# Optimization experiments

Hardware: AMD Instinct MI355X
Metric: run time of the kernel (lower is better)

Reference implementation:

```python
import jax, jax.numpy as jnp
import numpy as np

N_NODES = 100000
N_EDGES = 600000
IN_C, HID_C, OUT_C = 128, 128, 64


def gcn_conv(x, W, b, src, dst, n_nodes):
    """PyG GCNConv: out = D^{-1/2} (A + I) D^{-1/2} X W + b (symmetric norm, self-loops)."""
    h = x @ W  # [N, C_out] transform first (as PyG does)
    # add self loops
    loop = jnp.arange(n_nodes, dtype=src.dtype)
    s = jnp.concatenate([src, loop])
    d = jnp.concatenate([dst, loop])
    # degree over targets (edge weight = 1)
    deg = jax.ops.segment_sum(jnp.ones_like(d, dtype=h.dtype), d, num_segments=n_nodes)
    dinv = jnp.where(deg > 0, jax.lax.rsqrt(deg), 0.0)
    norm = dinv[s] * dinv[d]  # [E+N]
    msg = h[s] * norm[:, None]  # gather + scale
    out = jax.ops.segment_sum(msg, d, num_segments=n_nodes)  # scatter-add
    return out + b


def setup_inputs() -> dict:
    key = jax.random.key(0)
    k1, k2, k3, k4, k5 = jax.random.split(key, 5)
    x = jax.random.normal(k1, (N_NODES, IN_C), dtype=jnp.float32)
    src = jax.random.randint(k2, (N_EDGES,), 0, N_NODES, dtype=jnp.int32)
    dst = jax.random.randint(k3, (N_EDGES,), 0, N_NODES, dtype=jnp.int32)
    # Glorot-style init for conv weights, zero bias (PyG defaults)
    W1 = jax.random.normal(k4, (IN_C, HID_C), dtype=jnp.float32) * (1.0 / np.sqrt(IN_C))
    W2 = jax.random.normal(k5, (HID_C, OUT_C), dtype=jnp.float32) * (1.0 / np.sqrt(HID_C))
    b1 = jnp.zeros((HID_C,), dtype=jnp.float32)
    b2 = jnp.zeros((OUT_C,), dtype=jnp.float32)
    return {"x": x, "W1": W1, "b1": b1, "W2": W2, "b2": b2, "src": src, "dst": dst}


def reference(x, W1, b1, W2, b2, src, dst):
    h = gcn_conv(x, W1, b1, src, dst, N_NODES)
    h = jax.nn.relu(h)
    out = gcn_conv(h, W2, b2, src, dst, N_NODES)
    return out
```

## Files before the change

### kernel.cpp

```cpp
#include <hip/hip_runtime.h>
#include <math.h>


typedef __bf16 bf16x8 __attribute__((ext_vector_type(8)));
typedef float f32x4 __attribute__((ext_vector_type(4)));

constexpr int CAP = 32;

union ABu {
  unsigned short u16[8];
  uint4 u4;
  bf16x8 v;
};

__device__ inline unsigned short f2bf(float f) {
  unsigned u = __float_as_uint(f);
  return (unsigned short)((u + 0x7fffu + ((u >> 16) & 1u)) >> 16);
}

__device__ inline void unpack8(uint4 v, float* f) {
  f[0] = __uint_as_float(v.x << 16);
  f[1] = __uint_as_float(v.x & 0xffff0000u);
  f[2] = __uint_as_float(v.y << 16);
  f[3] = __uint_as_float(v.y & 0xffff0000u);
  f[4] = __uint_as_float(v.z << 16);
  f[5] = __uint_as_float(v.z & 0xffff0000u);
  f[6] = __uint_as_float(v.w << 16);
  f[7] = __uint_as_float(v.w & 0xffff0000u);
}

__device__ inline uint4 pack8(const float* a) {
  uint4 o;
  o.x = (unsigned)f2bf(a[0]) | ((unsigned)f2bf(a[1]) << 16);
  o.y = (unsigned)f2bf(a[2]) | ((unsigned)f2bf(a[3]) << 16);
  o.z = (unsigned)f2bf(a[4]) | ((unsigned)f2bf(a[5]) << 16);
  o.w = (unsigned)f2bf(a[6]) | ((unsigned)f2bf(a[7]) << 16);
  return o;
}

__global__ __launch_bounds__(256) void k_pre(const float* __restrict__ W1,
                                             const float* __restrict__ W2,
                                             unsigned short* __restrict__ Wb1,
                                             unsigned short* __restrict__ Wb2,
                                             int* __restrict__ counts, int n) {
  constexpr int CONV_BLOCKS = (128 * 128 + 128 * 64) / 256;
  if (blockIdx.x < CONV_BLOCKS) {
    int idx = blockIdx.x * 256 + threadIdx.x;
    if (idx < 128 * 128) {
      int k = idx >> 7, c = idx & 127;
      Wb1[(((k >> 3) << 7) + c) * 8 + (k & 7)] = f2bf(W1[idx]);
    } else {
      int j = idx - 128 * 128;
      int k = j >> 6, c = j & 63;
      Wb2[(((k >> 3) << 6) + c) * 8 + (k & 7)] = f2bf(W2[j]);
    }
    return;
  }
  int i = (blockIdx.x - CONV_BLOCKS) * 256 + threadIdx.x;
  if (i < n) counts[i] = 0;
}


__device__ inline void slot_body(const int* __restrict__ src,
                                 const int* __restrict__ dst,
                                 int* __restrict__ counts,
                                 int* __restrict__ eslot, int E, int bid) {
  int base = (bid * 256 + (int)threadIdx.x) * 8;
  if (base + 7 < E) {
    int4 d0 = *(const int4*)(dst + base);
    int4 d1 = *(const int4*)(dst + base + 4);
    int4 s0 = *(const int4*)(src + base);
    int4 s1 = *(const int4*)(src + base + 4);
    int r0 = atomicAdd(&counts[d0.x], 1);
    int r1 = atomicAdd(&counts[d0.y], 1);
    int r2 = atomicAdd(&counts[d0.z], 1);
    int r3 = atomicAdd(&counts[d0.w], 1);
    int r4 = atomicAdd(&counts[d1.x], 1);
    int r5 = atomicAdd(&counts[d1.y], 1);
    int r6 = atomicAdd(&counts[d1.z], 1);
    int r7 = atomicAdd(&counts[d1.w], 1);
    r0 = r0 < CAP - 1 ? r0 : CAP - 1;
    r1 = r1 < CAP - 1 ? r1 : CAP - 1;
    r2 = r2 < CAP - 1 ? r2 : CAP - 1;
    r3 = r3 < CAP - 1 ? r3 : CAP - 1;
    r4 = r4 < CAP - 1 ? r4 : CAP - 1;
    r5 = r5 < CAP - 1 ? r5 : CAP - 1;
    r6 = r6 < CAP - 1 ? r6 : CAP - 1;
    r7 = r7 < CAP - 1 ? r7 : CAP - 1;
    eslot[(size_t)d0.x * CAP + r0] = s0.x;
    eslot[(size_t)d0.y * CAP + r1] = s0.y;
    eslot[(size_t)d0.z * CAP + r2] = s0.z;
    eslot[(size_t)d0.w * CAP + r3] = s0.w;
    eslot[(size_t)d1.x * CAP + r4] = s1.x;
    eslot[(size_t)d1.y * CAP + r5] = s1.y;
    eslot[(size_t)d1.z * CAP + r6] = s1.z;
    eslot[(size_t)d1.w * CAP + r7] = s1.w;
  } else {
    for (int e = base; e < E; ++e) {
      int dd = dst[e];
      int r = atomicAdd(&counts[dd], 1);
      r = r < CAP - 1 ? r : CAP - 1;
      eslot[(size_t)dd * CAP + r] = src[e];
    }
  }
}

__device__ inline void gemm1_body(const float* __restrict__ X,
                                  const unsigned short* __restrict__ Wb,
                                  unsigned short* __restrict__ Cb, int M,
                                  int rowblk) {
  constexpr int K = 128, N = 128, NT = N / 16, KS = K / 32;
  const int tid = threadIdx.x;
  const int wave = tid >> 6;
  const int lane = tid & 63;
  const int q = lane >> 4;
  const int l15 = lane & 15;
  const int row0 = rowblk * 64 + wave * 16;
  const int rowA = row0 + l15;

  f32x4 zero = {0.0f, 0.0f, 0.0f, 0.0f};
  f32x4 acc[NT];
#pragma unroll
  for (int t = 0; t < NT; ++t) acc[t] = zero;

#pragma unroll
  for (int kk = 0; kk < KS; ++kk) {
    ABu a;
    float4 f0 = make_float4(0.f, 0.f, 0.f, 0.f);
    float4 f1 = make_float4(0.f, 0.f, 0.f, 0.f);
    if (rowA < M) {
      const float4* ap = (const float4*)(X + (size_t)rowA * K + kk * 32 + q * 8);
      f0 = ap[0];
      f1 = ap[1];
    }
    a.u16[0] = f2bf(f0.x); a.u16[1] = f2bf(f0.y);
    a.u16[2] = f2bf(f0.z); a.u16[3] = f2bf(f0.w);
    a.u16[4] = f2bf(f1.x); a.u16[5] = f2bf(f1.y);
    a.u16[6] = f2bf(f1.z); a.u16[7] = f2bf(f1.w);
#pragma unroll
    for (int nt = 0; nt < NT; ++nt) {
      ABu b;
      b.u4 = *(const uint4*)(Wb + ((size_t)(kk * 4 + q) * N + nt * 16 + l15) * 8);
      acc[nt] = __builtin_amdgcn_mfma_f32_16x16x32_bf16(a.v, b.v, acc[nt], 0, 0, 0);
    }
  }

#pragma unroll
  for (int v = 0; v < 4; ++v) {
    int row = row0 + q * 4 + v;
    if (row < M) {
#pragma unroll
      for (int nt = 0; nt < NT; ++nt)
        Cb[(size_t)row * N + nt * 16 + l15] = f2bf(acc[nt][v]);
    }
  }
}

__global__ __launch_bounds__(256) void k_slot_gemm1(
    const int* __restrict__ src, const int* __restrict__ dst,
    int* __restrict__ counts, int* __restrict__ eslot, int E, int EB,
    const float* __restrict__ X, const unsigned short* __restrict__ Wb1,
    unsigned short* __restrict__ h1, int M) {
  if ((int)blockIdx.x < EB)
    slot_body(src, dst, counts, eslot, E, blockIdx.x);
  else
    gemm1_body(X, Wb1, h1, M, blockIdx.x - EB);
}

__global__ __launch_bounds__(256) void k_dinv(const int* __restrict__ counts,
                                              float* __restrict__ dinv, int n) {
  int i = blockIdx.x * 256 + threadIdx.x;
  if (i < n) dinv[i] = rsqrtf((float)(counts[i] + 1));
}

__global__ __launch_bounds__(256) void k_aggemm(const unsigned short* __restrict__ h1,
                                                const float* __restrict__ dinv,
                                                const float* __restrict__ b1,
                                                const int* __restrict__ counts,
                                                const int* __restrict__ eslot,
                                                const unsigned short* __restrict__ Wb2,
                                                unsigned short* __restrict__ h2s,
                                                int n) {
  constexpr int LDA = 136;
  __shared__ unsigned short As[16 * LDA];
  __shared__ float sdinv[16];
  const int tid = threadIdx.x;

  {
    const int nl = tid >> 4;
    const int q = tid & 15;
    const int node = blockIdx.x * 16 + nl;
    float acc[8];
    if (node < n) {
      const uint4* h4 = (const uint4*)h1;
      float di = dinv[node];
      if (q == 0) sdinv[nl] = di;
      unpack8(h4[(size_t)node * 16 + q], acc);
#pragma unroll
      for (int j = 0; j < 8; ++j) acc[j] *= di;

      int cnt = counts[node];
      if (cnt > CAP) cnt = CAP;
      const int* sl = eslot + (size_t)node * CAP;
      if (cnt > 0) {
        int lim = cnt < 16 ? cnt : 16;
        int my_s = sl[q < lim ? q : 0];
        float my_dv = dinv[my_s];
        for (int e = 0; e < lim; e += 8) {
          int idx[8];
          float dv[8];
#pragma unroll
          for (int i = 0; i < 8; ++i) {
            idx[i] = __shfl(my_s, e + i, 16);
            float dl = __shfl(my_dv, e + i, 16);
            dv[i] = (e + i < lim) ? dl : 0.f;
          }
          uint4 rr[8];
#pragma unroll
          for (int i = 0; i < 8; ++i) rr[i] = h4[(size_t)idx[i] * 16 + q];
#pragma unroll
          for (int i = 0; i < 8; ++i) {
            float g[8];
            unpack8(rr[i], g);
#pragma unroll
            for (int j = 0; j < 8; ++j) acc[j] = fmaf(g[j], dv[i], acc[j]);
          }
        }
        if (cnt > 16) {
          int rem = cnt - 16;
          int my_s2 = sl[16 + (q < rem ? q : 0)];
          float my_dv2 = dinv[my_s2];
          for (int e = 0; e < rem; e += 8) {
            int idx[8];
            float dv[8];
#pragma unroll
            for (int i = 0; i < 8; ++i) {
              idx[i] = __shfl(my_s2, e + i, 16);
              float dl = __shfl(my_dv2, e + i, 16);
              dv[i] = (e + i < rem) ? dl : 0.f;
            }
            uint4 rr[8];
#pragma unroll
            for (int i = 0; i < 8; ++i) rr[i] = h4[(size_t)idx[i] * 16 + q];
#pragma unroll
            for (int i = 0; i < 8; ++i) {
              float g[8];
              unpack8(rr[i], g);
#pragma unroll
              for (int j = 0; j < 8; ++j) acc[j] = fmaf(g[j], dv[i], acc[j]);
            }
          }
        }
      }
      const float4* b14 = (const float4*)b1;
      float4 ba = b14[q * 2], bb = b14[q * 2 + 1];
      float bias[8] = {ba.x, ba.y, ba.z, ba.w, bb.x, bb.y, bb.z, bb.w};
#pragma unroll
      for (int i = 0; i < 8; ++i) acc[i] = fmaxf(fmaf(acc[i], di, bias[i]), 0.f);
    } else {
      if (q == 0) sdinv[nl] = 0.f;
#pragma unroll
      for (int i = 0; i < 8; ++i) acc[i] = 0.f;
    }
    *(uint4*)&As[nl * LDA + q * 8] = pack8(acc);
  }
  __syncthreads();

  {
    const int wave = tid >> 6;
    const int lane = tid & 63;
    const int q = lane >> 4;
    const int l15 = lane & 15;
    f32x4 acc = {0.0f, 0.0f, 0.0f, 0.0f};
#pragma unroll
    for (int kk = 0; kk < 4; ++kk) {
      ABu a, b;
      a.u4 = *(const uint4*)&As[l15 * LDA + kk * 32 + q * 8];
      b.u4 = *(const uint4*)(Wb2 + ((size_t)(kk * 4 + q) * 64 + wave * 16 + l15) * 8);
      acc = __builtin_amdgcn_mfma_f32_16x16x32_bf16(a.v, b.v, acc, 0, 0, 0);
    }
#pragma unroll
    for (int v = 0; v < 4; ++v) {
      int rl = q * 4 + v;
      int row = blockIdx.x * 16 + rl;
      if (row < n) h2s[(size_t)row * 64 + wave * 16 + l15] = f2bf(acc[v] * sdinv[rl]);
    }
  }
}

__global__ __launch_bounds__(256) void k_agg2(const unsigned short* __restrict__ h2s,
                                              const float* __restrict__ dinv,
                                              const float* __restrict__ b2,
                                              const int* __restrict__ counts,
                                              const int* __restrict__ eslot,
                                              float* __restrict__ out, int n) {
  constexpr int CQ = 8;
  const int tid = threadIdx.x;
  const int node = blockIdx.x * 32 + tid / CQ;
  const int q = tid % CQ;
  if (node >= n) return;

  const uint4* h4 = (const uint4*)h2s;
  float di = dinv[node];
  float acc[8];
  unpack8(h4[(size_t)node * CQ + q], acc);

  int cnt = counts[node];
  if (cnt > CAP) cnt = CAP;
  const int* sl = eslot + (size_t)node * CAP;
  for (int b = 0; b * 8 < cnt; ++b) {
    int rem = cnt - b * 8;
    int lim = rem < 8 ? rem : 8;
    int my_s = sl[b * 8 + (q < lim ? q : 0)];
    int idx[8];
#pragma unroll
    for (int i = 0; i < 8; ++i) idx[i] = __shfl(my_s, i, 8);
    uint4 rr[8];
#pragma unroll
    for (int i = 0; i < 8; ++i) rr[i] = h4[(size_t)idx[i] * CQ + q];
#pragma unroll
    for (int i = 0; i < 8; ++i) {
      float w = (i < lim) ? 1.f : 0.f;
      float g[8];
      unpack8(rr[i], g);
#pragma unroll
      for (int j = 0; j < 8; ++j) acc[j] = fmaf(g[j], w, acc[j]);
    }
  }

  const float4* b24 = (const float4*)b2;
  float4 ba = b24[q * 2], bb = b24[q * 2 + 1];
  float bias[8] = {ba.x, ba.y, ba.z, ba.w, bb.x, bb.y, bb.z, bb.w};
  float4 o0, o1;
  o0.x = fmaf(acc[0], di, bias[0]);
  o0.y = fmaf(acc[1], di, bias[1]);
  o0.z = fmaf(acc[2], di, bias[2]);
  o0.w = fmaf(acc[3], di, bias[3]);
  o1.x = fmaf(acc[4], di, bias[4]);
  o1.y = fmaf(acc[5], di, bias[5]);
  o1.z = fmaf(acc[6], di, bias[6]);
  o1.w = fmaf(acc[7], di, bias[7]);
  ((float4*)out)[(size_t)node * 16 + q * 2 + 0] = o0;
  ((float4*)out)[(size_t)node * 16 + q * 2 + 1] = o1;
}


extern "C" void kernel_launch(void* const* d_in, const int* in_sizes, int n_in,
                              void* d_out, int out_size, void* d_ws, size_t ws_size,
                              hipStream_t stream) {
  const float* x  = (const float*)d_in[0];
  const float* W1 = (const float*)d_in[1];
  const float* b1 = (const float*)d_in[2];
  const float* W2 = (const float*)d_in[3];
  const float* b2 = (const float*)d_in[4];
  const int* src  = (const int*)d_in[5];
  const int* dst  = (const int*)d_in[6];
  float* out = (float*)d_out;

  constexpr int IN_C = 128, HID_C = 128, OUT_C = 64;
  const int N = in_sizes[0] / IN_C;
  const int E = in_sizes[5];

  char* p = (char*)d_ws;
  auto alloc = [&](size_t bytes) {
    char* r = p;
    p += (bytes + 255) & ~(size_t)255;
    return r;
  };
  float* dinv    = (float*)alloc((size_t)N * 4);
  int*   counts  = (int*)alloc((size_t)N * 4);
  int*   eslot   = (int*)alloc((size_t)N * CAP * 4);
  unsigned short* Wb1 = (unsigned short*)alloc((size_t)IN_C * HID_C * 2);
  unsigned short* Wb2 = (unsigned short*)alloc((size_t)HID_C * OUT_C * 2);
  unsigned short* h1  = (unsigned short*)alloc((size_t)N * HID_C * 2);
  unsigned short* h2s = (unsigned short*)alloc((size_t)N * OUT_C * 2);

  const int T = 256;
  const int EB8 = ((E + 7) / 8 + T - 1) / T;
  const int RB_TOTAL = (N + 63) / 64;
  constexpr int CONV_BLOCKS = (128 * 128 + 128 * 64) / 256;

  k_pre<<<CONV_BLOCKS + (N + T - 1) / T, T, 0, stream>>>(W1, W2, Wb1, Wb2, counts, N);
  k_slot_gemm1<<<EB8 + RB_TOTAL, T, 0, stream>>>(src, dst, counts, eslot, E, EB8,
                                                 x, Wb1, h1, N);
  k_dinv<<<(N + T - 1) / T, T, 0, stream>>>(counts, dinv, N);
  k_aggemm<<<(N + 15) / 16, T, 0, stream>>>(h1, dinv, b1, counts, eslot, Wb2, h2s, N);
  k_agg2<<<(N + 31) / 32, T, 0, stream>>>(h2s, dinv, b2, counts, eslot, out, N);
}
```

Before: 202.5 us.

## Build per-node edge slots with LDS histograms in 128 scanning blocks

Replaces the global-atomic edge bucketing with 128 blocks. Each block owns a contiguous range of destination nodes, scans the whole dst array, and counts edges into a shared-memory histogram using LDS atomics. The same blocks then write counts and dinv directly, which removes the counts zeroing in k_pre and the separate k_dinv launch. The cost is that every scanning block reads the full edge list, so total reads grow about 128-fold and are likely served from L2. That extra traffic may outweigh the savings from avoiding global atomic contention.

```diff
diff --git a/kernel.cpp b/kernel.cpp
--- a/kernel.cpp
+++ b/kernel.cpp
@@ -6,6 +6,7 @@
 typedef float f32x4 __attribute__((ext_vector_type(4)));
 
 constexpr int CAP = 32;
+constexpr int NB_SCAN = 128;
 
 union ABu {
   unsigned short u16[8];
@@ -41,67 +42,78 @@
 __global__ __launch_bounds__(256) void k_pre(const float* __restrict__ W1,
                                              const float* __restrict__ W2,
                                              unsigned short* __restrict__ Wb1,
-                                             unsigned short* __restrict__ Wb2,
-                                             int* __restrict__ counts, int n) {
-  constexpr int CONV_BLOCKS = (128 * 128 + 128 * 64) / 256;
-  if (blockIdx.x < CONV_BLOCKS) {
-    int idx = blockIdx.x * 256 + threadIdx.x;
-    if (idx < 128 * 128) {
-      int k = idx >> 7, c = idx & 127;
-      Wb1[(((k >> 3) << 7) + c) * 8 + (k & 7)] = f2bf(W1[idx]);
-    } else {
-      int j = idx - 128 * 128;
-      int k = j >> 6, c = j & 63;
-      Wb2[(((k >> 3) << 6) + c) * 8 + (k & 7)] = f2bf(W2[j]);
-    }
-    return;
-  }
-  int i = (blockIdx.x - CONV_BLOCKS) * 256 + threadIdx.x;
-  if (i < n) counts[i] = 0;
-}
-
-
-__device__ inline void slot_body(const int* __restrict__ src,
+                                             unsigned short* __restrict__ Wb2) {
+  int idx = blockIdx.x * 256 + threadIdx.x;
+  if (idx < 128 * 128) {
+    int k = idx >> 7, c = idx & 127;
+    Wb1[(((k >> 3) << 7) + c) * 8 + (k & 7)] = f2bf(W1[idx]);
+  } else {
+    int j = idx - 128 * 128;
+    int k = j >> 6, c = j & 63;
+    Wb2[(((k >> 3) << 6) + c) * 8 + (k & 7)] = f2bf(W2[j]);
+  }
+}
+
+
+__device__ inline void scan_body(const int* __restrict__ src,
                                  const int* __restrict__ dst,
                                  int* __restrict__ counts,
-                                 int* __restrict__ eslot, int E, int bid) {
-  int base = (bid * 256 + (int)threadIdx.x) * 8;
-  if (base + 7 < E) {
-    int4 d0 = *(const int4*)(dst + base);
-    int4 d1 = *(const int4*)(dst + base + 4);
-    int4 s0 = *(const int4*)(src + base);
-    int4 s1 = *(const int4*)(src + base + 4);
-    int r0 = atomicAdd(&counts[d0.x], 1);
-    int r1 = atomicAdd(&counts[d0.y], 1);
-    int r2 = atomicAdd(&counts[d0.z], 1);
-    int r3 = atomicAdd(&counts[d0.w], 1);
-    int r4 = atomicAdd(&counts[d1.x], 1);
-    int r5 = atomicAdd(&counts[d1.y], 1);
-    int r6 = atomicAdd(&counts[d1.z], 1);
-    int r7 = atomicAdd(&counts[d1.w], 1);
-    r0 = r0 < CAP - 1 ? r0 : CAP - 1;
-    r1 = r1 < CAP - 1 ? r1 : CAP - 1;
-    r2 = r2 < CAP - 1 ? r2 : CAP - 1;
-    r3 = r3 < CAP - 1 ? r3 : CAP - 1;
-    r4 = r4 < CAP - 1 ? r4 : CAP - 1;
-    r5 = r5 < CAP - 1 ? r5 : CAP - 1;
-    r6 = r6 < CAP - 1 ? r6 : CAP - 1;
-    r7 = r7 < CAP - 1 ? r7 : CAP - 1;
-    eslot[(size_t)d0.x * CAP + r0] = s0.x;
-    eslot[(size_t)d0.y * CAP + r1] = s0.y;
-    eslot[(size_t)d0.z * CAP + r2] = s0.z;
-    eslot[(size_t)d0.w * CAP + r3] = s0.w;
-    eslot[(size_t)d1.x * CAP + r4] = s1.x;
-    eslot[(size_t)d1.y * CAP + r5] = s1.y;
-    eslot[(size_t)d1.z * CAP + r6] = s1.z;
-    eslot[(size_t)d1.w * CAP + r7] = s1.w;
-  } else {
-    for (int e = base; e < E; ++e) {
-      int dd = dst[e];
-      int r = atomicAdd(&counts[dd], 1);
-      r = r < CAP - 1 ? r : CAP - 1;
-      eslot[(size_t)dd * CAP + r] = src[e];
-    }
+                                 float* __restrict__ dinv,
+                                 int* __restrict__ eslot,
+                                 int E, int N, int bid, int* hist) {
+  const int per = (N + NB_SCAN - 1) / NB_SCAN;
+  const int base = bid * per;
+  int lim = N - base;
+  lim = lim < per ? lim : per;
+  if (lim < 0) lim = 0;
+  for (int i = threadIdx.x; i < lim; i += 256) hist[i] = 0;
+  __syncthreads();
+
+  const int4* d4 = (const int4*)dst;
+  const int nv = E >> 2;
+  for (int v = threadIdx.x; v < nv; v += 256) {
+    int4 d = d4[v];
+    int e0 = v << 2;
+    unsigned r;
+    r = (unsigned)(d.x - base);
+    if (r < (unsigned)lim) {
+      int rk = atomicAdd(&hist[r], 1);
+      rk = rk < CAP - 1 ? rk : CAP - 1;
+      eslot[(size_t)d.x * CAP + rk] = src[e0 + 0];
+    }
+    r = (unsigned)(d.y - base);
+    if (r < (unsigned)lim) {
+      int rk = atomicAdd(&hist[r], 1);
+      rk = rk < CAP - 1 ? rk : CAP - 1;
+      eslot[(size_t)d.y * CAP + rk] = src[e0 + 1];
+    }
+    r = (unsigned)(d.z - base);
+    if (r < (unsigned)lim) {
+      int rk = atomicAdd(&hist[r], 1);
+      rk = rk < CAP - 1 ? rk : CAP - 1;
+      eslot[(size_t)d.z * CAP + rk] = src[e0 + 2];
+    }
+    r = (unsigned)(d.w - base);
+    if (r < (unsigned)lim) {
+      int rk = atomicAdd(&hist[r], 1);
+      rk = rk < CAP - 1 ? rk : CAP - 1;
+      eslot[(size_t)d.w * CAP + rk] = src[e0 + 3];
+    }
+  }
+  for (int e = (nv << 2) + (int)threadIdx.x; e < E; e += 256) {
+    int dd = dst[e];
+    unsigned r = (unsigned)(dd - base);
+    if (r < (unsigned)lim) {
+      int rk = atomicAdd(&hist[r], 1);
+      rk = rk < CAP - 1 ? rk : CAP - 1;
+      eslot[(size_t)dd * CAP + rk] = src[e];
+    }
+  }
+  __syncthreads();
+  for (int i = threadIdx.x; i < lim; i += 256) {
+    int c = hist[i];
+    counts[base + i] = c;
+    dinv[base + i] = rsqrtf((float)(c + 1));
   }
 }
 
@@ -156,21 +168,17 @@
   }
 }
 
-__global__ __launch_bounds__(256) void k_slot_gemm1(
+__global__ __launch_bounds__(256) void k_scan_gemm1(
     const int* __restrict__ src, const int* __restrict__ dst,
-    int* __restrict__ counts, int* __restrict__ eslot, int E, int EB,
+    int* __restrict__ counts, float* __restrict__ dinv,
+    int* __restrict__ eslot, int E, int N,
     const float* __restrict__ X, const unsigned short* __restrict__ Wb1,
     unsigned short* __restrict__ h1, int M) {
-  if ((int)blockIdx.x < EB)
-    slot_body(src, dst, counts, eslot, E, blockIdx.x);
+  __shared__ int hist[1024];
+  if ((int)blockIdx.x < NB_SCAN)
+    scan_body(src, dst, counts, dinv, eslot, E, N, blockIdx.x, hist);
   else
-    gemm1_body(X, Wb1, h1, M, blockIdx.x - EB);
-}
-
-__global__ __launch_bounds__(256) void k_dinv(const int* __restrict__ counts,
-                                              float* __restrict__ dinv, int n) {
-  int i = blockIdx.x * 256 + threadIdx.x;
-  if (i < n) dinv[i] = rsqrtf((float)(counts[i] + 1));
+    gemm1_body(X, Wb1, h1, M, blockIdx.x - NB_SCAN);
 }
 
 __global__ __launch_bounds__(256) void k_aggemm(const unsigned short* __restrict__ h1,
@@ -376,14 +384,12 @@
   unsigned short* h2s = (unsigned short*)alloc((size_t)N * OUT_C * 2);
 
   const int T = 256;
-  const int EB8 = ((E + 7) / 8 + T - 1) / T;
   const int RB_TOTAL = (N + 63) / 64;
   constexpr int CONV_BLOCKS = (128 * 128 + 128 * 64) / 256;
 
-  k_pre<<<CONV_BLOCKS + (N + T - 1) / T, T, 0, stream>>>(W1, W2, Wb1, Wb2, counts, N);
-  k_slot_gemm1<<<EB8 + RB_TOTAL, T, 0, stream>>>(src, dst, counts, eslot, E, EB8,
-                                                 x, Wb1, h1, N);
-  k_dinv<<<(N + T - 1) / T, T, 0, stream>>>(counts, dinv, N);
+  k_pre<<<CONV_BLOCKS, T, 0, stream>>>(W1, W2, Wb1, Wb2);
+  k_scan_gemm1<<<NB_SCAN + RB_TOTAL, T, 0, stream>>>(src, dst, counts, dinv, eslot,
+                                                     E, N, x, Wb1, h1, N);
   k_aggemm<<<(N + 15) / 16, T, 0, stream>>>(h1, dinv, b1, counts, eslot, Wb2, h2s, N);
   k_agg2<<<(N + 31) / 32, T, 0, stream>>>(h2s, dinv, b2, counts, eslot, out, N);
 }
```

After: 463.2 us. +128.7%, slower.

## Replace global per-node atomics with two-pass binned edge bucketing

Applied to the files above, without the earlier changes.

Edge slotting no longer uses a global atomic per edge on the per-node counts array. Edges are first bucketed into 1024-node bins using shared-memory histograms plus one global atomic per bin per block. A second kernel then builds each bin's slot lists and degree/dinv with shared-memory atomics. This removes the zeroing of counts and the separate dinv kernel, but adds a pass that writes and re-reads an int2 bin buffer. Bin overflow past CAPB silently drops edges, so bounds clamps were added to the aggregation kernels.

```diff
diff --git a/kernel.cpp b/kernel.cpp
--- a/kernel.cpp
+++ b/kernel.cpp
@@ -6,6 +6,7 @@
 typedef float f32x4 __attribute__((ext_vector_type(4)));
 
 constexpr int CAP = 32;
+constexpr int CAPB = 8192;
 
 union ABu {
   unsigned short u16[8];
@@ -42,65 +43,70 @@
                                              const float* __restrict__ W2,
                                              unsigned short* __restrict__ Wb1,
                                              unsigned short* __restrict__ Wb2,
-                                             int* __restrict__ counts, int n) {
+                                             int* __restrict__ gCur, int nbins) {
   constexpr int CONV_BLOCKS = (128 * 128 + 128 * 64) / 256;
-  if (blockIdx.x < CONV_BLOCKS) {
-    int idx = blockIdx.x * 256 + threadIdx.x;
-    if (idx < 128 * 128) {
-      int k = idx >> 7, c = idx & 127;
-      Wb1[(((k >> 3) << 7) + c) * 8 + (k & 7)] = f2bf(W1[idx]);
-    } else {
-      int j = idx - 128 * 128;
-      int k = j >> 6, c = j & 63;
-      Wb2[(((k >> 3) << 6) + c) * 8 + (k & 7)] = f2bf(W2[j]);
-    }
+  if (blockIdx.x == CONV_BLOCKS) {
+    if ((int)threadIdx.x < nbins) gCur[threadIdx.x] = 0;
     return;
   }
-  int i = (blockIdx.x - CONV_BLOCKS) * 256 + threadIdx.x;
-  if (i < n) counts[i] = 0;
-}
-
-
-__device__ inline void slot_body(const int* __restrict__ src,
+  int idx = blockIdx.x * 256 + threadIdx.x;
+  if (idx < 128 * 128) {
+    int k = idx >> 7, c = idx & 127;
+    Wb1[(((k >> 3) << 7) + c) * 8 + (k & 7)] = f2bf(W1[idx]);
+  } else {
+    int j = idx - 128 * 128;
+    int k = j >> 6, c = j & 63;
+    Wb2[(((k >> 3) << 6) + c) * 8 + (k & 7)] = f2bf(W2[j]);
+  }
+}
+
+
+__device__ inline void binA_body(const int* __restrict__ src,
                                  const int* __restrict__ dst,
-                                 int* __restrict__ counts,
-                                 int* __restrict__ eslot, int E, int bid) {
-  int base = (bid * 256 + (int)threadIdx.x) * 8;
+                                 int* __restrict__ gCur,
+                                 int2* __restrict__ binBuf,
+                                 int E, int nbins, int bid,
+                                 int* bc, int* bbase) {
+  const int tid = threadIdx.x;
+  if (tid < 128) bc[tid] = 0;
+  __syncthreads();
+  int base = (bid * 256 + tid) * 8;
+  int ds[8], ss[8];
+  bool vl[8];
   if (base + 7 < E) {
     int4 d0 = *(const int4*)(dst + base);
     int4 d1 = *(const int4*)(dst + base + 4);
     int4 s0 = *(const int4*)(src + base);
     int4 s1 = *(const int4*)(src + base + 4);
-    int r0 = atomicAdd(&counts[d0.x], 1);
-    int r1 = atomicAdd(&counts[d0.y], 1);
-    int r2 = atomicAdd(&counts[d0.z], 1);
-    int r3 = atomicAdd(&counts[d0.w], 1);
-    int r4 = atomicAdd(&counts[d1.x], 1);
-    int r5 = atomicAdd(&counts[d1.y], 1);
-    int r6 = atomicAdd(&counts[d1.z], 1);
-    int r7 = atomicAdd(&counts[d1.w], 1);
-    r0 = r0 < CAP - 1 ? r0 : CAP - 1;
-    r1 = r1 < CAP - 1 ? r1 : CAP - 1;
-    r2 = r2 < CAP - 1 ? r2 : CAP - 1;
-    r3 = r3 < CAP - 1 ? r3 : CAP - 1;
-    r4 = r4 < CAP - 1 ? r4 : CAP - 1;
-    r5 = r5 < CAP - 1 ? r5 : CAP - 1;
-    r6 = r6 < CAP - 1 ? r6 : CAP - 1;
-    r7 = r7 < CAP - 1 ? r7 : CAP - 1;
-    eslot[(size_t)d0.x * CAP + r0] = s0.x;
-    eslot[(size_t)d0.y * CAP + r1] = s0.y;
-    eslot[(size_t)d0.z * CAP + r2] = s0.z;
-    eslot[(size_t)d0.w * CAP + r3] = s0.w;
-    eslot[(size_t)d1.x * CAP + r4] = s1.x;
-    eslot[(size_t)d1.y * CAP + r5] = s1.y;
-    eslot[(size_t)d1.z * CAP + r6] = s1.z;
-    eslot[(size_t)d1.w * CAP + r7] = s1.w;
+    ds[0] = d0.x; ds[1] = d0.y; ds[2] = d0.z; ds[3] = d0.w;
+    ds[4] = d1.x; ds[5] = d1.y; ds[6] = d1.z; ds[7] = d1.w;
+    ss[0] = s0.x; ss[1] = s0.y; ss[2] = s0.z; ss[3] = s0.w;
+    ss[4] = s1.x; ss[5] = s1.y; ss[6] = s1.z; ss[7] = s1.w;
+#pragma unroll
+    for (int i = 0; i < 8; ++i) vl[i] = true;
   } else {
-    for (int e = base; e < E; ++e) {
-      int dd = dst[e];
-      int r = atomicAdd(&counts[dd], 1);
-      r = r < CAP - 1 ? r : CAP - 1;
-      eslot[(size_t)dd * CAP + r] = src[e];
+#pragma unroll
+    for (int i = 0; i < 8; ++i) {
+      int e = base + i;
+      bool v = e < E;
+      int ee = v ? e : E - 1;
+      ds[i] = dst[ee]; ss[i] = src[ee]; vl[i] = v;
+    }
+  }
+#pragma unroll
+  for (int i = 0; i < 8; ++i)
+    if (vl[i]) atomicAdd(&bc[ds[i] >> 10], 1);
+  __syncthreads();
+  if (tid < nbins) bbase[tid] = atomicAdd(&gCur[tid], bc[tid]);
+  __syncthreads();
+  if (tid < 128) bc[tid] = 0;
+  __syncthreads();
+#pragma unroll
+  for (int i = 0; i < 8; ++i) {
+    if (vl[i]) {
+      int b = ds[i] >> 10;
+      int pos = bbase[b] + atomicAdd(&bc[b], 1);
+      if (pos < CAPB) binBuf[(size_t)b * CAPB + pos] = make_int2(ss[i], ds[i]);
     }
   }
 }
@@ -156,21 +162,46 @@
   }
 }
 
-__global__ __launch_bounds__(256) void k_slot_gemm1(
+__global__ __launch_bounds__(256) void k_binA_gemm1(
     const int* __restrict__ src, const int* __restrict__ dst,
-    int* __restrict__ counts, int* __restrict__ eslot, int E, int EB,
-    const float* __restrict__ X, const unsigned short* __restrict__ Wb1,
+    int* __restrict__ gCur, int2* __restrict__ binBuf, int E, int nbins,
+    int EB, const float* __restrict__ X, const unsigned short* __restrict__ Wb1,
     unsigned short* __restrict__ h1, int M) {
+  __shared__ int bc[128];
+  __shared__ int bbase[128];
   if ((int)blockIdx.x < EB)
-    slot_body(src, dst, counts, eslot, E, blockIdx.x);
+    binA_body(src, dst, gCur, binBuf, E, nbins, blockIdx.x, bc, bbase);
   else
     gemm1_body(X, Wb1, h1, M, blockIdx.x - EB);
 }
 
-__global__ __launch_bounds__(256) void k_dinv(const int* __restrict__ counts,
-                                              float* __restrict__ dinv, int n) {
-  int i = blockIdx.x * 256 + threadIdx.x;
-  if (i < n) dinv[i] = rsqrtf((float)(counts[i] + 1));
+__global__ __launch_bounds__(256) void k_binB(const int2* __restrict__ binBuf,
+                                              const int* __restrict__ gCur,
+                                              int* __restrict__ counts,
+                                              float* __restrict__ dinv,
+                                              int* __restrict__ eslot, int N) {
+  __shared__ int hist[1024];
+  const int b = blockIdx.x;
+  const int base = b << 10;
+  int lim = N - base;
+  lim = lim < 1024 ? lim : 1024;
+  for (int i = threadIdx.x; i < 1024; i += 256) hist[i] = 0;
+  __syncthreads();
+  int cnt = gCur[b];
+  cnt = cnt < CAPB ? cnt : CAPB;
+  const int2* bb = binBuf + (size_t)b * CAPB;
+  for (int i = threadIdx.x; i < cnt; i += 256) {
+    int2 pr = bb[i];
+    int rk = atomicAdd(&hist[pr.y - base], 1);
+    rk = rk < CAP - 1 ? rk : CAP - 1;
+    eslot[(size_t)pr.y * CAP + rk] = pr.x;
+  }
+  __syncthreads();
+  for (int i = threadIdx.x; i < lim; i += 256) {
+    int c = hist[i];
+    counts[base + i] = c;
+    dinv[base + i] = rsqrtf((float)(c + 1));
+  }
 }
 
 __global__ __launch_bounds__(256) void k_aggemm(const unsigned short* __restrict__ h1,
@@ -205,6 +236,7 @@
       if (cnt > 0) {
         int lim = cnt < 16 ? cnt : 16;
         int my_s = sl[q < lim ? q : 0];
+        if ((unsigned)my_s >= (unsigned)n) my_s = 0;
         float my_dv = dinv[my_s];
         for (int e = 0; e < lim; e += 8) {
           int idx[8];
@@ -229,6 +261,7 @@
         if (cnt > 16) {
           int rem = cnt - 16;
           int my_s2 = sl[16 + (q < rem ? q : 0)];
+          if ((unsigned)my_s2 >= (unsigned)n) my_s2 = 0;
           float my_dv2 = dinv[my_s2];
           for (int e = 0; e < rem; e += 8) {
             int idx[8];
@@ -312,6 +345,7 @@
     int rem = cnt - b * 8;
     int lim = rem < 8 ? rem : 8;
     int my_s = sl[b * 8 + (q < lim ? q : 0)];
+    if ((unsigned)my_s >= (unsigned)n) my_s = 0;
     int idx[8];
 #pragma unroll
     for (int i = 0; i < 8; ++i) idx[i] = __shfl(my_s, i, 8);
@@ -360,6 +394,7 @@
   constexpr int IN_C = 128, HID_C = 128, OUT_C = 64;
   const int N = in_sizes[0] / IN_C;
   const int E = in_sizes[5];
+  const int nbins = (N + 1023) >> 10;
 
   char* p = (char*)d_ws;
   auto alloc = [&](size_t bytes) {
@@ -367,6 +402,8 @@
     p += (bytes + 255) & ~(size_t)255;
     return r;
   };
+  int*   gCur    = (int*)alloc((size_t)nbins * 4);
+  int2*  binBuf  = (int2*)alloc((size_t)nbins * CAPB * 8);
   float* dinv    = (float*)alloc((size_t)N * 4);
   int*   counts  = (int*)alloc((size_t)N * 4);
   int*   eslot   = (int*)alloc((size_t)N * CAP * 4);
@@ -380,10 +417,10 @@
   const int RB_TOTAL = (N + 63) / 64;
   constexpr int CONV_BLOCKS = (128 * 128 + 128 * 64) / 256;
 
-  k_pre<<<CONV_BLOCKS + (N + T - 1) / T, T, 0, stream>>>(W1, W2, Wb1, Wb2, counts, N);
-  k_slot_gemm1<<<EB8 + RB_TOTAL, T, 0, stream>>>(src, dst, counts, eslot, E, EB8,
-                                                 x, Wb1, h1, N);
-  k_dinv<<<(N + T - 1) / T, T, 0, stream>>>(counts, dinv, N);
+  k_pre<<<CONV_BLOCKS + 1, T, 0, stream>>>(W1, W2, Wb1, Wb2, gCur, nbins);
+  k_binA_gemm1<<<EB8 + RB_TOTAL, T, 0, stream>>>(src, dst, gCur, binBuf, E, nbins,
+                                                 EB8, x, Wb1, h1, N);
+  k_binB<<<nbins, T, 0, stream>>>(binBuf, gCur, counts, dinv, eslot, N);
   k_aggemm<<<(N + 15) / 16, T, 0, stream>>>(h1, dinv, b1, counts, eslot, Wb2, h2s, N);
   k_agg2<<<(N + 31) / 32, T, 0, stream>>>(h2s, dinv, b2, counts, eslot, out, N);
 }
```

Result: faster. 188.3 us (-7.0%).
